# Optimization experiments

Measured on AMD Instinct MI355X. Metric: run time of the kernel, lower is better.

Reference implementation:

```python
import jax, jax.numpy as jnp
import numpy as np

NEG_CLAMP = -100.0  # torch BCE clamps log terms at -100


def cxcywh_to_xyxy(b):
    cx, cy, w, h = b[..., 0], b[..., 1], b[..., 2], b[..., 3]
    return jnp.stack([cx - 0.5 * w, cy - 0.5 * h, cx + 0.5 * w, cy + 0.5 * h], axis=-1)


def generalized_box_iou(a, b):
    # a: [N,4], b: [T,4] in xyxy
    area_a = (a[:, 2] - a[:, 0]) * (a[:, 3] - a[:, 1])
    area_b = (b[:, 2] - b[:, 0]) * (b[:, 3] - b[:, 1])
    lt = jnp.maximum(a[:, None, :2], b[None, :, :2])
    rb = jnp.minimum(a[:, None, 2:], b[None, :, 2:])
    wh = jnp.clip(rb - lt, 0.0)
    inter = wh[..., 0] * wh[..., 1]
    union = area_a[:, None] + area_b[None, :] - inter
    iou = inter / union
    ltc = jnp.minimum(a[:, None, :2], b[None, :, :2])
    rbc = jnp.maximum(a[:, None, 2:], b[None, :, 2:])
    whc = jnp.clip(rbc - ltc, 0.0)
    areac = whc[..., 0] * whc[..., 1]
    return iou - (areac - union) / areac


def setup_inputs() -> dict:
    key = jax.random.key(0)
    k0, k1, k2, k3, k4, k5 = jax.random.split(key, 6)
    bs, Q, C = 4, 300, 80
    T = 200  # 50 targets per image
    H = W = 160
    H2 = W2 = 320
    pred_logits = jax.random.normal(k0, (bs, Q, C), dtype=jnp.float32)
    pred_boxes = jax.random.uniform(k1, (bs, Q, 4), dtype=jnp.float32, minval=0.02, maxval=0.98)
    pred_masks = jax.random.normal(k2, (bs, Q, H, W), dtype=jnp.float32)
    tgt_ids = jax.random.randint(k3, (T,), 0, C)
    tgt_bbox = jax.random.uniform(k4, (T, 4), dtype=jnp.float32, minval=0.02, maxval=0.98)
    tgt_masks = jnp.round(jax.random.uniform(k5, (T, H2, W2), dtype=jnp.float32))  # binary masks
    return {"pred_logits": pred_logits, "pred_boxes": pred_boxes, "pred_masks": pred_masks,
            "tgt_ids": tgt_ids, "tgt_bbox": tgt_bbox, "tgt_masks": tgt_masks}


def reference(pred_logits, pred_boxes, pred_masks, tgt_ids, tgt_bbox, tgt_masks):
    cost_class_w, cost_bbox_w, cost_giou_w, cost_mask_w, cost_dice_w = 2.0, 5.0, 2.0, 2.0, 2.0
    bs, Q = pred_logits.shape[:2]
    N = bs * Q
    T = tgt_bbox.shape[0]

    out_prob = jax.nn.sigmoid(pred_logits.reshape(N, -1))      # [N, C]
    out_bbox = pred_boxes.reshape(N, 4)

    cost_class = -out_prob[:, tgt_ids]                           # [N, T] gather
    cost_bbox = jnp.abs(out_bbox[:, None, :] - tgt_bbox[None, :, :]).sum(-1)  # L1 cdist
    cost_giou = -generalized_box_iou(cxcywh_to_xyxy(out_bbox), cxcywh_to_xyxy(tgt_bbox))

    C = cost_bbox_w * cost_bbox + cost_giou_w * cost_giou + cost_class_w * cost_class

    # mask costs
    H, W = pred_masks.shape[-2:]
    HW = H * W
    out_logits = pred_masks.reshape(N, HW)
    out_flat = jax.nn.sigmoid(out_logits)                        # [N, HW]
    tgt_resized = jax.image.resize(tgt_masks, (T, H, W), method='bilinear')  # align_corners=False
    tgt_flat = tgt_resized.reshape(T, HW)

    numerator = 2.0 * (out_flat @ tgt_flat.T)                    # [N, T]
    denominator = out_flat.sum(-1)[:, None] + tgt_flat.sum(-1)[None, :]
    cost_dice = -(numerator + 1.0) / (jnp.clip(denominator, 1e-6) + 1.0)

    # BCE mean over pixels as pairwise matmuls (same math as the expanded torch version)
    log_p = jnp.maximum(jax.nn.log_sigmoid(out_logits), NEG_CLAMP)       # log(p)
    log_1mp = jnp.maximum(jax.nn.log_sigmoid(-out_logits), NEG_CLAMP)    # log(1-p)
    cost_mask = -(log_p @ tgt_flat.T + log_1mp @ (1.0 - tgt_flat).T) / HW

    C = C + cost_mask_w * cost_mask + cost_dice_w * cost_dice
    return C.reshape(bs, Q, T)
```

## Files before the change

kernel.cpp:

```cpp
#include <hip/hip_runtime.h>
#include <math.h>

#define N_PRED 1200
#define N_TGT  200
#define T_PAD  208
#define NCLS   80
#define W_OUT  160
#define W_IN   320
#define HW     25600
#define K_TOT  25600
#define KS     40
#define K_CHUNK 640
#define BK     64
#define MT     19
#define PROW   (2 * T_PAD)


typedef __bf16 bf16x8 __attribute__((ext_vector_type(8)));
typedef float  f32x4  __attribute__((ext_vector_type(4)));

__device__ __forceinline__ unsigned short f2bf(float f) {
    unsigned int u = __float_as_uint(f);
    u = u + 0x7FFFu + ((u >> 16) & 1u);
    return (unsigned short)(u >> 16);
}

#if __has_builtin(__builtin_amdgcn_cvt_pk_bf16_f32)
typedef __bf16 bf16x2 __attribute__((ext_vector_type(2)));
__device__ __forceinline__ unsigned pk_bf16(float a, float b) {
    bf16x2 v = __builtin_amdgcn_cvt_pk_bf16_f32(a, b);
    return *(unsigned*)&v;
}
#else
__device__ __forceinline__ unsigned pk_bf16(float a, float b) {
    return (unsigned)f2bf(a) | ((unsigned)f2bf(b) << 16);
}
#endif

__device__ __forceinline__ void taps(int i, int& i0, float w[4]) {
    if (i == 0)            { i0 = 0;       w[0]=3.f/7.f; w[1]=3.f/7.f; w[2]=1.f/7.f; w[3]=0.f; }
    else if (i == W_OUT-1) { i0 = 2*i - 2; w[0]=0.f;     w[1]=1.f/7.f; w[2]=3.f/7.f; w[3]=3.f/7.f; }
    else                   { i0 = 2*i - 1; w[0]=0.125f;  w[1]=0.375f;  w[2]=0.375f;  w[3]=0.125f; }
}

__global__ void prep_kernel(const float* __restrict__ tm,
                            unsigned short* __restrict__ tgt_bf,
                            float* __restrict__ tgt_sumP,
                            float* __restrict__ sig_rs,
                            float* __restrict__ l1p_rs) {
    const int t = blockIdx.y, q = blockIdx.x, tid = threadIdx.x;
    if (t >= N_TGT) {
        uint4 z = make_uint4(0,0,0,0);
        uint4* dst = (uint4*)(tgt_bf + (size_t)t * HW) + q * (HW/8/4);
        for (int u = tid; u < HW/8/4; u += 256) dst[u] = z;
        if (q == 0) {
            const int base = (t - N_TGT) * 150;
            if (tid < 150) { sig_rs[base + tid] = 0.f; l1p_rs[base + tid] = 0.f; }
        }
        if (tid == 0) tgt_sumP[q * T_PAD + t] = 0.f;
        return;
    }
    const float* src = tm + (size_t)t * (W_IN * W_IN);
    float part = 0.f;
    const int p0 = q * (HW/4);
    for (int pp = tid; pp < HW/4; pp += 256) {
        const int p = p0 + pp;
        const int i = p / W_OUT, j = p % W_OUT;
        int r0, c0; float wr[4], wc[4];
        taps(i, r0, wr); taps(j, c0, wc);
        float v = 0.f;
        #pragma unroll
        for (int a = 0; a < 4; a++) {
            const float* row = src + (size_t)(r0 + a) * W_IN + c0;
            float h = wc[0]*row[0] + wc[1]*row[1] + wc[2]*row[2] + wc[3]*row[3];
            v += wr[a] * h;
        }
        tgt_bf[(size_t)t * HW + p] = f2bf(v);
        part += v;
    }
    __shared__ float red[256];
    red[tid] = part; __syncthreads();
    for (int s = 128; s > 0; s >>= 1) { if (tid < s) red[tid] += red[tid + s]; __syncthreads(); }
    if (tid == 0) tgt_sumP[q * T_PAD + t] = red[0];
}

#define DECL13(p) f32x4 p##0={0,0,0,0}, p##1={0,0,0,0}, p##2={0,0,0,0}, p##3={0,0,0,0}, \
    p##4={0,0,0,0}, p##5={0,0,0,0}, p##6={0,0,0,0}, p##7={0,0,0,0}, p##8={0,0,0,0}, \
    p##9={0,0,0,0}, p##10={0,0,0,0}, p##11={0,0,0,0}, p##12={0,0,0,0}

#define STEP(tt) { bf16x8 b = *(const bf16x8*)&ldsB[((tt)*16 + l16) * 64 + co]; \
    accS##tt = __builtin_amdgcn_mfma_f32_16x16x32_bf16(aS, b, accS##tt, 0, 0, 0); \
    accX##tt = __builtin_amdgcn_mfma_f32_16x16x32_bf16(aX, b, accX##tt, 0, 0, 0); }

#define CONVW(J, RA) { \
    const float x0 = RA.x, x1 = RA.y, x2 = RA.z, x3 = RA.w; \
    const float e0 = __expf(-x0), e1 = __expf(-x1), e2 = __expf(-x2), e3 = __expf(-x3); \
    const float u0 = 1.f + e0, u1 = 1.f + e1, u2 = 1.f + e2, u3 = 1.f + e3; \
    const float s0 = __builtin_amdgcn_rcpf(u0), s1 = __builtin_amdgcn_rcpf(u1); \
    const float s2 = __builtin_amdgcn_rcpf(u2), s3 = __builtin_amdgcn_rcpf(u3); \
    sS##J += (s0 + s1) + (s2 + s3); \
    sL##J -= (x0 + __logf(u0)) + (x1 + __logf(u1)) + (x2 + __logf(u2)) + (x3 + __logf(u3)); \
    const int rl_ = (J)*16 + arow; \
    const int ao_ = rl_*64 + (((ac >> 1) ^ (rl_ & 7)) * 8) + (ac & 1) * 4; \
    *(uint2*)&ldsAX[ao_] = make_uint2(pk_bf16(x0, x1), pk_bf16(x2, x3)); \
    *(uint2*)&ldsAS[ao_] = make_uint2(pk_bf16(s0, s1), pk_bf16(s2, s3)); }

#define BADDR(U) ((((U) >> 3) * 64) + (((((U) & 7)) ^ (((U) >> 3) & 7)) * 8))

#define EPI(tt) { const size_t b0 = base + (size_t)(wave * 16 + quad * 4) * PROW + 2 * ((tt) * 16 + l16); \
    *(float2*)&P[b0           ] = make_float2(accS##tt[0], accX##tt[0]); \
    *(float2*)&P[b0 +     PROW] = make_float2(accS##tt[1], accX##tt[1]); \
    *(float2*)&P[b0 + 2 * PROW] = make_float2(accS##tt[2], accX##tt[2]); \
    *(float2*)&P[b0 + 3 * PROW] = make_float2(accS##tt[3], accX##tt[3]); }

__global__ __launch_bounds__(256, 2)
void gemm_kernel(const float* __restrict__ pm,
                 const unsigned short* __restrict__ tgt_bf,
                 float* __restrict__ P,
                 float* __restrict__ sig_rs, float* __restrict__ l1p_rs) {
    const int ks = blockIdx.x, mtile = blockIdx.y;
    const int tid = threadIdx.x;
    const int wave = tid >> 6, lane = tid & 63;
    const int quad = lane >> 4, l16 = lane & 15;
    const int l7 = l16 & 7;

    __shared__ unsigned short ldsAX[64 * 64];
    __shared__ unsigned short ldsAS[64 * 64];
    __shared__ unsigned short ldsB[T_PAD * 64];

    DECL13(accS);
    DECL13(accX);
    float sS0 = 0.f, sS1 = 0.f, sS2 = 0.f, sS3 = 0.f;
    float sL0 = 0.f, sL1 = 0.f, sL2 = 0.f, sL3 = 0.f;

    const int m0 = mtile * 64;
    const int arow = tid >> 4;
    const int ac   = tid & 15;
    const int k0   = ks * K_CHUNK;

    int r0i = m0 + 0*16 + arow; if (r0i > N_PRED-1) r0i = N_PRED-1;
    int r1i = m0 + 1*16 + arow; if (r1i > N_PRED-1) r1i = N_PRED-1;
    int r2i = m0 + 2*16 + arow; if (r2i > N_PRED-1) r2i = N_PRED-1;
    int r3i = m0 + 3*16 + arow; if (r3i > N_PRED-1) r3i = N_PRED-1;
    const float* ap0 = pm + (size_t)r0i * K_TOT + ac * 4;
    const float* ap1 = pm + (size_t)r1i * K_TOT + ac * 4;
    const float* ap2 = pm + (size_t)r2i * K_TOT + ac * 4;
    const float* ap3 = pm + (size_t)r3i * K_TOT + ac * 4;

    const int bu = tid;

    float4 rA0 = *(const float4*)(ap0 + k0);
    float4 rA1 = *(const float4*)(ap1 + k0);
    float4 rA2 = *(const float4*)(ap2 + k0);
    float4 rA3 = *(const float4*)(ap3 + k0);
    uint4 rB0, rB1, rB2, rB3, rB4, rB5, rB6;
    {
        const unsigned short* bp = tgt_bf + k0;
        rB0 = *(const uint4*)(bp + (size_t)((bu       ) >> 3) * K_TOT + ((bu       ) & 7) * 8);
        rB1 = *(const uint4*)(bp + (size_t)((bu +  256) >> 3) * K_TOT + ((bu +  256) & 7) * 8);
        rB2 = *(const uint4*)(bp + (size_t)((bu +  512) >> 3) * K_TOT + ((bu +  512) & 7) * 8);
        rB3 = *(const uint4*)(bp + (size_t)((bu +  768) >> 3) * K_TOT + ((bu +  768) & 7) * 8);
        rB4 = *(const uint4*)(bp + (size_t)((bu + 1024) >> 3) * K_TOT + ((bu + 1024) & 7) * 8);
        rB5 = *(const uint4*)(bp + (size_t)((bu + 1280) >> 3) * K_TOT + ((bu + 1280) & 7) * 8);
        if (tid < 128)
            rB6 = *(const uint4*)(bp + (size_t)((bu + 1536) >> 3) * K_TOT + ((bu + 1536) & 7) * 8);
    }

    for (int ki = 0; ki < K_CHUNK / BK; ki++) {
        __syncthreads();
        CONVW(0, rA0); CONVW(1, rA1); CONVW(2, rA2); CONVW(3, rA3);
        *(uint4*)&ldsB[BADDR(bu       )] = rB0;
        *(uint4*)&ldsB[BADDR(bu +  256)] = rB1;
        *(uint4*)&ldsB[BADDR(bu +  512)] = rB2;
        *(uint4*)&ldsB[BADDR(bu +  768)] = rB3;
        *(uint4*)&ldsB[BADDR(bu + 1024)] = rB4;
        *(uint4*)&ldsB[BADDR(bu + 1280)] = rB5;
        if (tid < 128)
            *(uint4*)&ldsB[BADDR(bu + 1536)] = rB6;
        __syncthreads();
        if (ki != K_CHUNK / BK - 1) {
            const int kn = k0 + (ki + 1) * BK;
            rA0 = *(const float4*)(ap0 + kn);
            rA1 = *(const float4*)(ap1 + kn);
            rA2 = *(const float4*)(ap2 + kn);
            rA3 = *(const float4*)(ap3 + kn);
            const unsigned short* bp = tgt_bf + kn;
            rB0 = *(const uint4*)(bp + (size_t)((bu       ) >> 3) * K_TOT + ((bu       ) & 7) * 8);
            rB1 = *(const uint4*)(bp + (size_t)((bu +  256) >> 3) * K_TOT + ((bu +  256) & 7) * 8);
            rB2 = *(const uint4*)(bp + (size_t)((bu +  512) >> 3) * K_TOT + ((bu +  512) & 7) * 8);
            rB3 = *(const uint4*)(bp + (size_t)((bu +  768) >> 3) * K_TOT + ((bu +  768) & 7) * 8);
            rB4 = *(const uint4*)(bp + (size_t)((bu + 1024) >> 3) * K_TOT + ((bu + 1024) & 7) * 8);
            rB5 = *(const uint4*)(bp + (size_t)((bu + 1280) >> 3) * K_TOT + ((bu + 1280) & 7) * 8);
            if (tid < 128)
                rB6 = *(const uint4*)(bp + (size_t)((bu + 1536) >> 3) * K_TOT + ((bu + 1536) & 7) * 8);
        }
        #pragma unroll
        for (int kk = 0; kk < 2; kk++) {
            const int co = (((kk * 4 + quad) ^ l7)) * 8;
            bf16x8 aX = *(const bf16x8*)&ldsAX[(wave * 16 + l16) * 64 + co];
            bf16x8 aS = *(const bf16x8*)&ldsAS[(wave * 16 + l16) * 64 + co];
            STEP(0); STEP(1); STEP(2); STEP(3); STEP(4); STEP(5); STEP(6);
            STEP(7); STEP(8); STEP(9); STEP(10); STEP(11); STEP(12);
        }
    }
    const size_t base = ((size_t)(mtile * KS + ks)) * 64 * PROW;
    EPI(0); EPI(1); EPI(2); EPI(3); EPI(4); EPI(5); EPI(6);
    EPI(7); EPI(8); EPI(9); EPI(10); EPI(11); EPI(12);

    #pragma unroll
    for (int m = 1; m < 16; m <<= 1) {
        sS0 += __shfl_xor(sS0, m); sS1 += __shfl_xor(sS1, m);
        sS2 += __shfl_xor(sS2, m); sS3 += __shfl_xor(sS3, m);
        sL0 += __shfl_xor(sL0, m); sL1 += __shfl_xor(sL1, m);
        sL2 += __shfl_xor(sL2, m); sL3 += __shfl_xor(sL3, m);
    }
    if (l16 == 0) {
        const int rg0 = m0 + 0*16 + arow, rg1 = m0 + 1*16 + arow;
        const int rg2 = m0 + 2*16 + arow, rg3 = m0 + 3*16 + arow;
        if (rg0 < N_PRED) { atomicAdd(sig_rs + rg0, sS0); atomicAdd(l1p_rs + rg0, sL0); }
        if (rg1 < N_PRED) { atomicAdd(sig_rs + rg1, sS1); atomicAdd(l1p_rs + rg1, sL1); }
        if (rg2 < N_PRED) { atomicAdd(sig_rs + rg2, sS2); atomicAdd(l1p_rs + rg2, sL2); }
        if (rg3 < N_PRED) { atomicAdd(sig_rs + rg3, sS3); atomicAdd(l1p_rs + rg3, sL3); }
    }
}

__global__ void combine_kernel(const float* __restrict__ pred_logits,
                               const float* __restrict__ pred_boxes,
                               const int*   __restrict__ tgt_ids,
                               const float* __restrict__ tgt_bbox,
                               const float* __restrict__ P,
                               const float* __restrict__ sig_rs, const float* __restrict__ l1p_rs,
                               const float* __restrict__ tgt_sumP,
                               float* __restrict__ out) {
    const int e = blockIdx.x * 256 + threadIdx.x;
    if (e >= N_PRED * N_TGT) return;
    const int n = e / N_TGT, t = e - n * N_TGT;
    const int mtile = n >> 6, mrow = n & 63;

    const size_t pb = ((size_t)mtile * KS * 64 + mrow) * PROW + 2 * t;
    float s1 = 0.f, s2 = 0.f;
    for (int ks = 0; ks < KS; ks++) {
        float2 v = *(const float2*)&P[pb + (size_t)ks * 64 * PROW];
        s1 += v.x; s2 += v.y;
    }
    const float tsum = tgt_sumP[t] + tgt_sumP[T_PAD + t] + tgt_sumP[2*T_PAD + t] + tgt_sumP[3*T_PAD + t];
    const float denom = sig_rs[n] + tsum;
    const float cost_dice = -(2.f * s1 + 1.f) / (fmaxf(denom, 1e-6f) + 1.f);
    const float cost_mask = -(s2 + l1p_rs[n]) / (float)HW;
    const int id = tgt_ids[t];
    const float lg = pred_logits[(size_t)n * NCLS + id];
    const float p = 1.f / (1.f + __expf(-lg));
    const float4 ob = *(const float4*)(pred_boxes + (size_t)n * 4);
    const float4 tb = *(const float4*)(tgt_bbox + (size_t)t * 4);
    const float l1 = fabsf(ob.x - tb.x) + fabsf(ob.y - tb.y) + fabsf(ob.z - tb.z) + fabsf(ob.w - tb.w);
    const float ax0 = ob.x - 0.5f*ob.z, ay0 = ob.y - 0.5f*ob.w;
    const float ax1 = ob.x + 0.5f*ob.z, ay1 = ob.y + 0.5f*ob.w;
    const float bx0 = tb.x - 0.5f*tb.z, by0 = tb.y - 0.5f*tb.w;
    const float bx1 = tb.x + 0.5f*tb.z, by1 = tb.y + 0.5f*tb.w;
    const float areaA = (ax1 - ax0) * (ay1 - ay0);
    const float areaB = (bx1 - bx0) * (by1 - by0);
    const float iw = fmaxf(fminf(ax1, bx1) - fmaxf(ax0, bx0), 0.f);
    const float ih = fmaxf(fminf(ay1, by1) - fmaxf(ay0, by0), 0.f);
    const float inter = iw * ih;
    const float uni = areaA + areaB - inter;
    const float iou = inter / uni;
    const float cw = fmaxf(fmaxf(ax1, bx1) - fminf(ax0, bx0), 0.f);
    const float ch = fmaxf(fmaxf(ay1, by1) - fminf(ay0, by0), 0.f);
    const float areaC = cw * ch;
    const float giou = iou - (areaC - uni) / areaC;

    out[e] = 5.f * l1 + 2.f * (-giou) + 2.f * (-p) + 2.f * cost_mask + 2.f * cost_dice;
}

extern "C" void kernel_launch(void* const* d_in, const int* in_sizes, int n_in,
                              void* d_out, int out_size, void* d_ws, size_t ws_size,
                              hipStream_t stream) {
    const float* pred_logits = (const float*)d_in[0];
    const float* pred_boxes  = (const float*)d_in[1];
    const float* pred_masks  = (const float*)d_in[2];
    const int*   tgt_ids     = (const int*)d_in[3];
    const float* tgt_bbox    = (const float*)d_in[4];
    const float* tgt_masks   = (const float*)d_in[5];
    float* out = (float*)d_out;

    char* ws = (char*)d_ws;
    size_t off = 0;
    unsigned short* tgt_bf = (unsigned short*)(ws + off);
    off += (size_t)T_PAD * K_TOT * sizeof(unsigned short);
    off = (off + 255) & ~(size_t)255;
    float* tgt_sumP = (float*)(ws + off);
    float* sig_rs   = tgt_sumP + 4 * T_PAD;
    float* l1p_rs   = sig_rs + N_PRED;
    off += (size_t)(4 * T_PAD + 2 * N_PRED) * sizeof(float);
    off = (off + 255) & ~(size_t)255;
    float* P = (float*)(ws + off);
    off += (size_t)MT * KS * 64 * PROW * sizeof(float);

    hipLaunchKernelGGL(prep_kernel, dim3(4, T_PAD), dim3(256), 0, stream,
                       tgt_masks, tgt_bf, tgt_sumP, sig_rs, l1p_rs);
    hipLaunchKernelGGL(gemm_kernel, dim3(KS, MT), dim3(256), 0, stream,
                       pred_masks, tgt_bf, P, sig_rs, l1p_rs);
    hipLaunchKernelGGL(combine_kernel, dim3((N_PRED * N_TGT + 255) / 256), dim3(256), 0, stream,
                       pred_logits, pred_boxes, tgt_ids, tgt_bbox,
                       P, sig_rs, l1p_rs, tgt_sumP, out);
}
```

Baseline: 296.1 us.

## Load GEMM fragments directly from global memory into registers, bypassing LDS staging

The bf16 MFMA GEMM no longer stages the activation and target tiles through shared memory with barriers. Each lane now loads its own A row segment and B fragments straight from global memory in MFMA operand layout, converts them in registers, and software-pipelines the B loads between MFMA groups. This removes both __syncthreads per K step, the LDS writes and reads, and the shared-memory footprint. In exchange, each of the four waves re-reads the whole B tile from global memory, which adds redundant L1/L2 traffic through strided 16-byte loads, and register pressure goes up.

```diff
diff --git a/kernel.cpp b/kernel.cpp
--- a/kernel.cpp
+++ b/kernel.cpp
@@ -12,6 +12,7 @@
 #define KS     40
 #define K_CHUNK 640
 #define BK     64
+#define NI     (K_CHUNK / BK)
 #define MT     19
 #define PROW   (2 * T_PAD)
 
@@ -88,24 +89,29 @@
     p##4={0,0,0,0}, p##5={0,0,0,0}, p##6={0,0,0,0}, p##7={0,0,0,0}, p##8={0,0,0,0}, \
     p##9={0,0,0,0}, p##10={0,0,0,0}, p##11={0,0,0,0}, p##12={0,0,0,0}
 
-#define STEP(tt) { bf16x8 b = *(const bf16x8*)&ldsB[((tt)*16 + l16) * 64 + co]; \
-    accS##tt = __builtin_amdgcn_mfma_f32_16x16x32_bf16(aS, b, accS##tt, 0, 0, 0); \
-    accX##tt = __builtin_amdgcn_mfma_f32_16x16x32_bf16(aX, b, accX##tt, 0, 0, 0); }
-
-#define CONVW(J, RA) { \
-    const float x0 = RA.x, x1 = RA.y, x2 = RA.z, x3 = RA.w; \
-    const float e0 = __expf(-x0), e1 = __expf(-x1), e2 = __expf(-x2), e3 = __expf(-x3); \
-    const float u0 = 1.f + e0, u1 = 1.f + e1, u2 = 1.f + e2, u3 = 1.f + e3; \
-    const float s0 = __builtin_amdgcn_rcpf(u0), s1 = __builtin_amdgcn_rcpf(u1); \
-    const float s2 = __builtin_amdgcn_rcpf(u2), s3 = __builtin_amdgcn_rcpf(u3); \
-    sS##J += (s0 + s1) + (s2 + s3); \
-    sL##J -= (x0 + __logf(u0)) + (x1 + __logf(u1)) + (x2 + __logf(u2)) + (x3 + __logf(u3)); \
-    const int rl_ = (J)*16 + arow; \
-    const int ao_ = rl_*64 + (((ac >> 1) ^ (rl_ & 7)) * 8) + (ac & 1) * 4; \
-    *(uint2*)&ldsAX[ao_] = make_uint2(pk_bf16(x0, x1), pk_bf16(x2, x3)); \
-    *(uint2*)&ldsAS[ao_] = make_uint2(pk_bf16(s0, s1), pk_bf16(s2, s3)); }
-
-#define BADDR(U) ((((U) >> 3) * 64) + (((((U) & 7)) ^ (((U) >> 3) & 7)) * 8))
+#define LB(dst, tt, kof) dst = *(const uint4*)(bp + (tt)*16*K_TOT + (kof));
+
+#define MF(tt, BREG, AX, AS) { const bf16x8 bv = *(const bf16x8*)&BREG; \
+    accS##tt = __builtin_amdgcn_mfma_f32_16x16x32_bf16(AS, bv, accS##tt, 0, 0, 0); \
+    accX##tt = __builtin_amdgcn_mfma_f32_16x16x32_bf16(AX, bv, accX##tt, 0, 0, 0); }
+
+#define CONV8(A0, A1, FX, FS) { \
+    const float x0=A0.x, x1=A0.y, x2=A0.z, x3=A0.w; \
+    const float x4=A1.x, x5=A1.y, x6=A1.z, x7=A1.w; \
+    const float e0=__expf(-x0), e1=__expf(-x1), e2=__expf(-x2), e3=__expf(-x3); \
+    const float e4=__expf(-x4), e5=__expf(-x5), e6=__expf(-x6), e7=__expf(-x7); \
+    const float u0=1.f+e0, u1=1.f+e1, u2=1.f+e2, u3=1.f+e3; \
+    const float u4=1.f+e4, u5=1.f+e5, u6=1.f+e6, u7=1.f+e7; \
+    const float s0=__builtin_amdgcn_rcpf(u0), s1=__builtin_amdgcn_rcpf(u1); \
+    const float s2=__builtin_amdgcn_rcpf(u2), s3=__builtin_amdgcn_rcpf(u3); \
+    const float s4=__builtin_amdgcn_rcpf(u4), s5=__builtin_amdgcn_rcpf(u5); \
+    const float s6=__builtin_amdgcn_rcpf(u6), s7=__builtin_amdgcn_rcpf(u7); \
+    sS += ((s0+s1)+(s2+s3)) + ((s4+s5)+(s6+s7)); \
+    sL -= ((x0+__logf(u0)) + (x1+__logf(u1)) + (x2+__logf(u2)) + (x3+__logf(u3))) \
+        + ((x4+__logf(u4)) + (x5+__logf(u5)) + (x6+__logf(u6)) + (x7+__logf(u7))); \
+    uint4 tx = make_uint4(pk_bf16(x0,x1), pk_bf16(x2,x3), pk_bf16(x4,x5), pk_bf16(x6,x7)); \
+    uint4 ts = make_uint4(pk_bf16(s0,s1), pk_bf16(s2,s3), pk_bf16(s4,s5), pk_bf16(s6,s7)); \
+    FX = *(bf16x8*)&tx; FS = *(bf16x8*)&ts; }
 
 #define EPI(tt) { const size_t b0 = base + (size_t)(wave * 16 + quad * 4) * PROW + 2 * ((tt) * 16 + l16); \
     *(float2*)&P[b0           ] = make_float2(accS##tt[0], accX##tt[0]); \
@@ -122,105 +128,70 @@
     const int tid = threadIdx.x;
     const int wave = tid >> 6, lane = tid & 63;
     const int quad = lane >> 4, l16 = lane & 15;
-    const int l7 = l16 & 7;
-
-    __shared__ unsigned short ldsAX[64 * 64];
-    __shared__ unsigned short ldsAS[64 * 64];
-    __shared__ unsigned short ldsB[T_PAD * 64];
 
     DECL13(accS);
     DECL13(accX);
-    float sS0 = 0.f, sS1 = 0.f, sS2 = 0.f, sS3 = 0.f;
-    float sL0 = 0.f, sL1 = 0.f, sL2 = 0.f, sL3 = 0.f;
+    float sS = 0.f, sL = 0.f;
 
     const int m0 = mtile * 64;
-    const int arow = tid >> 4;
-    const int ac   = tid & 15;
-    const int k0   = ks * K_CHUNK;
-
-    int r0i = m0 + 0*16 + arow; if (r0i > N_PRED-1) r0i = N_PRED-1;
-    int r1i = m0 + 1*16 + arow; if (r1i > N_PRED-1) r1i = N_PRED-1;
-    int r2i = m0 + 2*16 + arow; if (r2i > N_PRED-1) r2i = N_PRED-1;
-    int r3i = m0 + 3*16 + arow; if (r3i > N_PRED-1) r3i = N_PRED-1;
-    const float* ap0 = pm + (size_t)r0i * K_TOT + ac * 4;
-    const float* ap1 = pm + (size_t)r1i * K_TOT + ac * 4;
-    const float* ap2 = pm + (size_t)r2i * K_TOT + ac * 4;
-    const float* ap3 = pm + (size_t)r3i * K_TOT + ac * 4;
-
-    const int bu = tid;
-
-    float4 rA0 = *(const float4*)(ap0 + k0);
-    float4 rA1 = *(const float4*)(ap1 + k0);
-    float4 rA2 = *(const float4*)(ap2 + k0);
-    float4 rA3 = *(const float4*)(ap3 + k0);
-    uint4 rB0, rB1, rB2, rB3, rB4, rB5, rB6;
-    {
-        const unsigned short* bp = tgt_bf + k0;
-        rB0 = *(const uint4*)(bp + (size_t)((bu       ) >> 3) * K_TOT + ((bu       ) & 7) * 8);
-        rB1 = *(const uint4*)(bp + (size_t)((bu +  256) >> 3) * K_TOT + ((bu +  256) & 7) * 8);
-        rB2 = *(const uint4*)(bp + (size_t)((bu +  512) >> 3) * K_TOT + ((bu +  512) & 7) * 8);
-        rB3 = *(const uint4*)(bp + (size_t)((bu +  768) >> 3) * K_TOT + ((bu +  768) & 7) * 8);
-        rB4 = *(const uint4*)(bp + (size_t)((bu + 1024) >> 3) * K_TOT + ((bu + 1024) & 7) * 8);
-        rB5 = *(const uint4*)(bp + (size_t)((bu + 1280) >> 3) * K_TOT + ((bu + 1280) & 7) * 8);
-        if (tid < 128)
-            rB6 = *(const uint4*)(bp + (size_t)((bu + 1536) >> 3) * K_TOT + ((bu + 1536) & 7) * 8);
-    }
-
-    for (int ki = 0; ki < K_CHUNK / BK; ki++) {
-        __syncthreads();
-        CONVW(0, rA0); CONVW(1, rA1); CONVW(2, rA2); CONVW(3, rA3);
-        *(uint4*)&ldsB[BADDR(bu       )] = rB0;
-        *(uint4*)&ldsB[BADDR(bu +  256)] = rB1;
-        *(uint4*)&ldsB[BADDR(bu +  512)] = rB2;
-        *(uint4*)&ldsB[BADDR(bu +  768)] = rB3;
-        *(uint4*)&ldsB[BADDR(bu + 1024)] = rB4;
-        *(uint4*)&ldsB[BADDR(bu + 1280)] = rB5;
-        if (tid < 128)
-            *(uint4*)&ldsB[BADDR(bu + 1536)] = rB6;
-        __syncthreads();
-        if (ki != K_CHUNK / BK - 1) {
-            const int kn = k0 + (ki + 1) * BK;
-            rA0 = *(const float4*)(ap0 + kn);
-            rA1 = *(const float4*)(ap1 + kn);
-            rA2 = *(const float4*)(ap2 + kn);
-            rA3 = *(const float4*)(ap3 + kn);
-            const unsigned short* bp = tgt_bf + kn;
-            rB0 = *(const uint4*)(bp + (size_t)((bu       ) >> 3) * K_TOT + ((bu       ) & 7) * 8);
-            rB1 = *(const uint4*)(bp + (size_t)((bu +  256) >> 3) * K_TOT + ((bu +  256) & 7) * 8);
-            rB2 = *(const uint4*)(bp + (size_t)((bu +  512) >> 3) * K_TOT + ((bu +  512) & 7) * 8);
-            rB3 = *(const uint4*)(bp + (size_t)((bu +  768) >> 3) * K_TOT + ((bu +  768) & 7) * 8);
-            rB4 = *(const uint4*)(bp + (size_t)((bu + 1024) >> 3) * K_TOT + ((bu + 1024) & 7) * 8);
-            rB5 = *(const uint4*)(bp + (size_t)((bu + 1280) >> 3) * K_TOT + ((bu + 1280) & 7) * 8);
-            if (tid < 128)
-                rB6 = *(const uint4*)(bp + (size_t)((bu + 1536) >> 3) * K_TOT + ((bu + 1536) & 7) * 8);
-        }
-        #pragma unroll
-        for (int kk = 0; kk < 2; kk++) {
-            const int co = (((kk * 4 + quad) ^ l7)) * 8;
-            bf16x8 aX = *(const bf16x8*)&ldsAX[(wave * 16 + l16) * 64 + co];
-            bf16x8 aS = *(const bf16x8*)&ldsAS[(wave * 16 + l16) * 64 + co];
-            STEP(0); STEP(1); STEP(2); STEP(3); STEP(4); STEP(5); STEP(6);
-            STEP(7); STEP(8); STEP(9); STEP(10); STEP(11); STEP(12);
-        }
-    }
+    const int k0 = ks * K_CHUNK;
+
+    const int rg = m0 + wave * 16 + l16;
+    int rowi = rg; if (rowi > N_PRED - 1) rowi = N_PRED - 1;
+    const float* ap = pm + (size_t)rowi * K_TOT + quad * 8;
+    const unsigned short* bp = tgt_bf + (size_t)l16 * K_TOT + quad * 8;
+
+    float4 A0 = *(const float4*)(ap + k0);
+    float4 A1 = *(const float4*)(ap + k0 + 4);
+    float4 A2 = *(const float4*)(ap + k0 + 32);
+    float4 A3 = *(const float4*)(ap + k0 + 36);
+    uint4 b0, b1, b2, b3, b4, b5, b6;
+    uint4 c0, c1, c2, c3, c4, c5;
+    LB(b0, 0, k0); LB(b1, 1, k0); LB(b2, 2, k0); LB(b3, 3, k0);
+    LB(b4, 4, k0); LB(b5, 5, k0); LB(b6, 6, k0);
+
+    for (int ki = 0; ki < NI; ki++) {
+        const int k = k0 + ki * BK;
+        bf16x8 aX0, aS0, aX1, aS1;
+        CONV8(A0, A1, aX0, aS0);
+        CONV8(A2, A3, aX1, aS1);
+        LB(c0, 7, k); LB(c1, 8, k); LB(c2, 9, k);
+        LB(c3, 10, k); LB(c4, 11, k); LB(c5, 12, k);
+        if (ki != NI - 1) {
+            A0 = *(const float4*)(ap + k + BK);
+            A1 = *(const float4*)(ap + k + BK + 4);
+            A2 = *(const float4*)(ap + k + BK + 32);
+            A3 = *(const float4*)(ap + k + BK + 36);
+        }
+        MF(0, b0, aX0, aS0); MF(1, b1, aX0, aS0); MF(2, b2, aX0, aS0);
+        MF(3, b3, aX0, aS0); MF(4, b4, aX0, aS0); MF(5, b5, aX0, aS0);
+        MF(6, b6, aX0, aS0);
+        LB(b0, 0, k + 32); LB(b1, 1, k + 32); LB(b2, 2, k + 32); LB(b3, 3, k + 32);
+        LB(b4, 4, k + 32); LB(b5, 5, k + 32); LB(b6, 6, k + 32);
+        MF(7, c0, aX0, aS0); MF(8, c1, aX0, aS0); MF(9, c2, aX0, aS0);
+        MF(10, c3, aX0, aS0); MF(11, c4, aX0, aS0); MF(12, c5, aX0, aS0);
+        LB(c0, 7, k + 32); LB(c1, 8, k + 32); LB(c2, 9, k + 32);
+        LB(c3, 10, k + 32); LB(c4, 11, k + 32); LB(c5, 12, k + 32);
+        MF(0, b0, aX1, aS1); MF(1, b1, aX1, aS1); MF(2, b2, aX1, aS1);
+        MF(3, b3, aX1, aS1); MF(4, b4, aX1, aS1); MF(5, b5, aX1, aS1);
+        MF(6, b6, aX1, aS1);
+        if (ki != NI - 1) {
+            LB(b0, 0, k + BK); LB(b1, 1, k + BK); LB(b2, 2, k + BK); LB(b3, 3, k + BK);
+            LB(b4, 4, k + BK); LB(b5, 5, k + BK); LB(b6, 6, k + BK);
+        }
+        MF(7, c0, aX1, aS1); MF(8, c1, aX1, aS1); MF(9, c2, aX1, aS1);
+        MF(10, c3, aX1, aS1); MF(11, c4, aX1, aS1); MF(12, c5, aX1, aS1);
+    }
+
     const size_t base = ((size_t)(mtile * KS + ks)) * 64 * PROW;
     EPI(0); EPI(1); EPI(2); EPI(3); EPI(4); EPI(5); EPI(6);
     EPI(7); EPI(8); EPI(9); EPI(10); EPI(11); EPI(12);
 
-    #pragma unroll
-    for (int m = 1; m < 16; m <<= 1) {
-        sS0 += __shfl_xor(sS0, m); sS1 += __shfl_xor(sS1, m);
-        sS2 += __shfl_xor(sS2, m); sS3 += __shfl_xor(sS3, m);
-        sL0 += __shfl_xor(sL0, m); sL1 += __shfl_xor(sL1, m);
-        sL2 += __shfl_xor(sL2, m); sL3 += __shfl_xor(sL3, m);
-    }
-    if (l16 == 0) {
-        const int rg0 = m0 + 0*16 + arow, rg1 = m0 + 1*16 + arow;
-        const int rg2 = m0 + 2*16 + arow, rg3 = m0 + 3*16 + arow;
-        if (rg0 < N_PRED) { atomicAdd(sig_rs + rg0, sS0); atomicAdd(l1p_rs + rg0, sL0); }
-        if (rg1 < N_PRED) { atomicAdd(sig_rs + rg1, sS1); atomicAdd(l1p_rs + rg1, sL1); }
-        if (rg2 < N_PRED) { atomicAdd(sig_rs + rg2, sS2); atomicAdd(l1p_rs + rg2, sL2); }
-        if (rg3 < N_PRED) { atomicAdd(sig_rs + rg3, sS3); atomicAdd(l1p_rs + rg3, sL3); }
+    sS += __shfl_xor(sS, 16); sS += __shfl_xor(sS, 32);
+    sL += __shfl_xor(sL, 16); sL += __shfl_xor(sL, 32);
+    if (quad == 0 && rg < N_PRED) {
+        atomicAdd(sig_rs + rg, sS);
+        atomicAdd(l1p_rs + rg, sL);
     }
 }
 
```

Measured after the change: 385.5 us. 30.2% more time.
